# Performance work log

Hardware: AMD Instinct MI355X
Metric: run time of the kernel (lower is better)

Reference implementation:

```python
import jax, jax.numpy as jnp
import numpy as np

B, N, C, K = 16, 2000, 4, 8
EPS = 1e-5


def setup_inputs() -> dict:
    key = jax.random.key(0)
    ks = jax.random.split(key, 10)
    def p(k, shape, s=0.1):
        return jax.random.normal(k, shape, jnp.float32) * s
    return {
        "data": jax.random.normal(ks[0], (B, 1, N, C), jnp.float32),
        "x": jax.random.normal(ks[1], (B, 1, N, 4), jnp.float32),
        "w1a": p(ks[2], (128, C)), "b1a": jnp.zeros((128,), jnp.float32),
        "w1b": p(ks[3], (128, 128)), "b1b": jnp.zeros((128,), jnp.float32),
        "w2": p(ks[4], (128, 2 * C + 2)), "b2": jnp.zeros((128,), jnp.float32),
        "res_wa": p(ks[5], (4, 128, 128)), "res_ba": jnp.zeros((4, 128), jnp.float32),
        "res_wb": p(ks[6], (4, 128, 128)), "res_bb": jnp.zeros((4, 128), jnp.float32),
        "wl": p(ks[7], (1, 128)), "bl": jnp.zeros((1,), jnp.float32),
    }


def conv1x1(t, w, b):
    # t: [B, Cin, H, W], w: [Cout, Cin]
    return jnp.einsum('bchw,oc->bohw', t, w) + b[None, :, None, None]


def bn(t):
    # training-mode BatchNorm2d, gamma=1 beta=0 (default init)
    m = jnp.mean(t, axis=(0, 2, 3), keepdims=True)
    v = jnp.var(t, axis=(0, 2, 3), keepdims=True)
    return (t - m) * jax.lax.rsqrt(v + EPS)


def instn(t):
    # InstanceNorm2d, affine=False
    m = jnp.mean(t, axis=(2, 3), keepdims=True)
    v = jnp.var(t, axis=(2, 3), keepdims=True)
    return (t - m) * jax.lax.rsqrt(v + EPS)


def res_block(t, wa, ba, wb, bb):
    h = jax.nn.relu(bn(instn(conv1x1(t, wa, ba))))
    h = bn(instn(conv1x1(h, wb, bb)))
    return jax.nn.relu(h + t)


def knn_idx(f, k):
    # f: [B, D, N]; negative squared distance, top-(k+1), drop self
    xx = jnp.sum(f * f, axis=1)                        # [B, N]
    inner = jnp.einsum('bdn,bdm->bnm', f, f)           # [B, N, N]
    pd = 2.0 * inner - xx[:, :, None] - xx[:, None, :]
    idx = jax.lax.top_k(pd, k + 1)[1]                  # [B, N, k+1]
    return idx[:, :, 1:]


def graph_feature(f, idx):
    # f: [B, D, N], idx: [B, N, k] -> [B, 2D, N, k]
    xf = jnp.transpose(f, (0, 2, 1))                   # [B, N, D]
    nb = jax.vmap(lambda a, i: a[i])(xf, idx)          # [B, N, k, D]
    xt = xf[:, :, None, :]
    gf = jnp.concatenate([jnp.broadcast_to(xt, nb.shape), xt - nb], axis=-1)
    return jnp.transpose(gf, (0, 3, 1, 2))


def reference(data, x, w1a, b1a, w1b, b1b, w2, b2,
              res_wa, res_ba, res_wb, res_bb, wl, bl):
    n = data.shape[2]
    t = jnp.transpose(data, (0, 3, 2, 1))              # [B, C, N, 1]

    # self_attention
    h = conv1x1(t, w1a, b1a)
    h = jax.nn.relu(bn(h))
    h = conv1x1(h, w1b, b1b)[..., 0]                   # [B, 128, N]
    h = h / (jnp.linalg.norm(h, axis=1, keepdims=True) + 1e-5)
    A_rowsum = jnp.einsum('bcn,bcm->bm', h, h)         # sum_i A[i, j]
    D = (A_rowsum - 1.0) / n                           # [B, N] (eye subtraction)
    feat = jnp.concatenate(
        [t, jax.nn.relu(jnp.tanh(D))[:, None, :, None]], axis=1)  # [B, C+1, N, 1]

    f = feat[..., 0]                                   # [B, C+1, N]
    idx = knn_idx(f, K)
    g = graph_feature(f, idx)                          # [B, 2C+2, N, K]

    out = jax.nn.relu(bn(conv1x1(g, w2, b2)))          # [B, 128, N, K]
    out = jnp.max(out, axis=-1, keepdims=True)         # [B, 128, N, 1]

    for i in range(4):
        out = res_block(out, res_wa[i], res_ba[i], res_wb[i], res_bb[i])

    logit = conv1x1(out, wl, bl)[:, 0, :, 0]           # [B, N]

    # weighted 8-point
    weights = jax.nn.relu(jnp.tanh(logit))             # [B, N]
    xp = jnp.transpose(x[:, 0], (0, 2, 1))             # [B, 4, N]
    ones = jnp.ones_like(xp[:, 0])
    X = jnp.stack([xp[:, 2] * xp[:, 0], xp[:, 2] * xp[:, 1], xp[:, 2],
                   xp[:, 3] * xp[:, 0], xp[:, 3] * xp[:, 1], xp[:, 3],
                   xp[:, 0], xp[:, 1], ones], axis=1)  # [B, 9, N]
    X = jnp.transpose(X, (0, 2, 1))                    # [B, N, 9]
    XwX = jnp.einsum('bnp,bnq->bpq', X, weights[:, :, None] * X)  # [B, 9, 9]
    _, v = jnp.linalg.eigh(XwX)                        # ascending eigvals
    e_hat = v[:, :, 0]                                 # smallest-eig eigenvector
    e_hat = e_hat / jnp.linalg.norm(e_hat, axis=1, keepdims=True)

    return (D, logit, e_hat)
```

## Files before the change

kernel.cpp:

```cpp
#include <hip/hip_runtime.h>
#include <math.h>

#define BB 16
#define NN 2000
#define CH 128
#define KNN 8
#define JCH 8
#define JSZ 250

__device__ inline float wred(float v) {
    for (int off = 32; off > 0; off >>= 1) v += __shfl_down(v, off, 64);
    return v;
}

__global__ void k_build_t(const float* __restrict__ data, float* __restrict__ t) {
    int i = blockIdx.x * 256 + threadIdx.x;
    if (i >= BB * 4 * NN) return;
    int n = i % NN;
    int c = (i / NN) & 3;
    int b = i / (4 * NN);
    t[i] = data[(b * NN + n) * 4 + c];
}

__global__ void k_conv1(const float* __restrict__ t, const float* __restrict__ w1a,
                        const float* __restrict__ b1a, float* __restrict__ c1) {
    int i = blockIdx.x * 256 + threadIdx.x;
    if (i >= BB * CH * NN) return;
    int n = i % NN;
    int rest = i / NN;
    int o = rest & 127;
    int b = rest >> 7;
    float acc = b1a[o];
    for (int c = 0; c < 4; ++c) acc += w1a[o * 4 + c] * t[(b * 4 + c) * NN + n];
    c1[i] = acc;
}

__global__ void k_chanstats(const float* __restrict__ src, float* __restrict__ chAB) {
    int o = blockIdx.x;
    int tid = threadIdx.x;
    float s = 0.f, ss = 0.f;
    for (int b = 0; b < BB; ++b) {
        const float* p = src + (b * CH + o) * NN;
        for (int n = tid; n < NN; n += 256) { float v = p[n]; s += v; ss += v * v; }
    }
    s = wred(s); ss = wred(ss);
    __shared__ float sh[8];
    int wid = tid >> 6, lane = tid & 63;
    if (lane == 0) { sh[wid] = s; sh[4 + wid] = ss; }
    __syncthreads();
    if (tid == 0) {
        float S0 = sh[0] + sh[1] + sh[2] + sh[3];
        float SS = sh[4] + sh[5] + sh[6] + sh[7];
        float m = S0 / (float)(BB * NN);
        float var = SS / (float)(BB * NN) - m * m;
        float a = rsqrtf(var + 1e-5f);
        chAB[o] = a;
        chAB[CH + o] = -m * a;
    }
}

__global__ __launch_bounds__(256) void k_gemm(const float* __restrict__ X, const float* __restrict__ W,
                                              const float* __restrict__ bias, float* __restrict__ Y,
                                              const float* __restrict__ ab, int mode) {
    int ot = blockIdx.x, by = blockIdx.y;
    int b = by >> 5, nt = by & 31;
    int n0 = nt * 64, o0 = ot * 64;
    int tid = threadIdx.x;
    int tx = tid & 15, ty = tid >> 4;
    __shared__ float Xs[32][64];
    __shared__ float Ws[32][68];
    float acc[4][4] = {};
    for (int jc = 0; jc < 4; ++jc) {
        for (int q = 0; q < 8; ++q) {
            int e = q * 256 + tid;
            int jj = e >> 6, nn = e & 63;
            int j = jc * 32 + jj, n = n0 + nn;
            float v = 0.f;
            if (n < NN) {
                v = X[(b * CH + j) * NN + n];
                if (mode == 1) v = fmaxf(ab[j] * v + ab[CH + j], 0.f);
                else if (mode == 2) { int bc = b * CH + j; v = fmaxf(ab[bc * 2] * v + ab[bc * 2 + 1], 0.f); }
            }
            Xs[jj][nn] = v;
        }
        for (int q = 0; q < 8; ++q) {
            int e = q * 256 + tid;
            int jj = e & 31, oo = e >> 5;
            Ws[jj][oo] = W[(o0 + oo) * CH + jc * 32 + jj];
        }
        __syncthreads();
        for (int jj = 0; jj < 32; ++jj) {
            float4 wv = *(const float4*)&Ws[jj][ty * 4];
            float4 xv = *(const float4*)&Xs[jj][tx * 4];
            float wva[4] = {wv.x, wv.y, wv.z, wv.w};
            float xva[4] = {xv.x, xv.y, xv.z, xv.w};
#pragma unroll
            for (int a = 0; a < 4; ++a)
#pragma unroll
                for (int bq = 0; bq < 4; ++bq) acc[a][bq] += wva[a] * xva[bq];
        }
        __syncthreads();
    }
    for (int a = 0; a < 4; ++a) {
        int o = o0 + ty * 4 + a;
        float bi = bias[o];
        for (int q = 0; q < 4; ++q) {
            int n = n0 + tx * 4 + q;
            if (n < NN) Y[(b * CH + o) * NN + n] = acc[a][q] + bi;
        }
    }
}

__global__ void k_invn(const float* __restrict__ h2, float* __restrict__ invn) {
    int b = blockIdx.x >> 3, chunk = blockIdx.x & 7;
    int n = chunk * 256 + threadIdx.x;
    if (n >= NN) return;
    float acc = 0.f;
    for (int c = 0; c < CH; ++c) { float v = h2[(b * CH + c) * NN + n]; acc += v * v; }
    invn[b * NN + n] = 1.f / (sqrtf(acc) + 1e-5f);
}

__global__ void k_S(const float* __restrict__ h2, const float* __restrict__ invn, float* __restrict__ Sv) {
    int row = blockIdx.x;
    int b = row >> 7;
    const float* p = h2 + row * NN;
    const float* iv = invn + b * NN;
    float s = 0.f;
    for (int n = threadIdx.x; n < NN; n += 256) s += p[n] * iv[n];
    s = wred(s);
    __shared__ float sh[4];
    int wid = threadIdx.x >> 6, lane = threadIdx.x & 63;
    if (lane == 0) sh[wid] = s;
    __syncthreads();
    if (threadIdx.x == 0) Sv[row] = sh[0] + sh[1] + sh[2] + sh[3];
}

__global__ void k_Df(const float* __restrict__ h2, const float* __restrict__ invn,
                     const float* __restrict__ Sv, const float* __restrict__ t,
                     float* __restrict__ outD, float* __restrict__ f5) {
    int b = blockIdx.x >> 3, chunk = blockIdx.x & 7;
    int n = chunk * 256 + threadIdx.x;
    if (n >= NN) return;
    float acc = 0.f;
    for (int c = 0; c < CH; ++c) acc += h2[(b * CH + c) * NN + n] * Sv[b * CH + c];
    float Ar = acc * invn[b * NN + n];
    float Dv = (Ar - 1.0f) / (float)NN;
    outD[b * NN + n] = Dv;
    for (int c = 0; c < 4; ++c) f5[(b * 5 + c) * NN + n] = t[(b * 4 + c) * NN + n];
    f5[(b * 5 + 4) * NN + n] = fmaxf(tanhf(Dv), 0.f);
}

__global__ __launch_bounds__(256) void k_knn_part(const float* __restrict__ f5,
                                                  float* __restrict__ pd, int* __restrict__ pj) {
    __shared__ float4 fs4[JSZ];
    __shared__ float fs1[JSZ];
    int jc = blockIdx.x, ic = blockIdx.y, b = blockIdx.z;
    int j0 = jc * JSZ;
    int tid = threadIdx.x;
    const float* fb = f5 + b * 5 * NN;
    for (int e = tid; e < JSZ; e += 256) {
        float4 v;
        v.x = fb[0 * NN + j0 + e];
        v.y = fb[1 * NN + j0 + e];
        v.z = fb[2 * NN + j0 + e];
        v.w = fb[3 * NN + j0 + e];
        fs4[e] = v;
        fs1[e] = fb[4 * NN + j0 + e];
    }
    __syncthreads();
    int i = ic * 256 + tid;
    if (i >= NN) return;
    float fi0 = fb[i], fi1 = fb[NN + i], fi2 = fb[2 * NN + i], fi3 = fb[3 * NN + i], fi4 = fb[4 * NN + i];
    float bd[8]; int bj[8];
#pragma unroll
    for (int q = 0; q < 8; ++q) { bd[q] = 1e30f; bj[q] = 0x7fffffff; }
    for (int jj = 0; jj < JSZ; ++jj) {
        float4 fj = fs4[jj];
        float fj4 = fs1[jj];
        int j = j0 + jj;
        float d0 = fi0 - fj.x, d1 = fi1 - fj.y, d2 = fi2 - fj.z;
        float d3 = fi3 - fj.w, d4 = fi4 - fj4;
        float d = d0 * d0 + d1 * d1 + d2 * d2 + d3 * d3 + d4 * d4;
        if (j != i && d < bd[7]) {
            float cd = d; int cj = j;
#pragma unroll
            for (int q = 0; q < 8; ++q) {
                bool lt = cd < bd[q];
                float td = lt ? bd[q] : cd;
                int tj = lt ? bj[q] : cj;
                bd[q] = lt ? cd : bd[q];
                bj[q] = lt ? cj : bj[q];
                cd = td; cj = tj;
            }
        }
    }
    long base = ((long)(b * NN + i) * JCH + jc) * 8;
#pragma unroll
    for (int q = 0; q < 8; ++q) { pd[base + q] = bd[q]; pj[base + q] = bj[q]; }
}

__global__ __launch_bounds__(256) void k_knn_merge(const float* __restrict__ pd, const int* __restrict__ pj,
                                                   int* __restrict__ idxb) {
    int s = blockIdx.x * 256 + threadIdx.x;
    if (s >= BB * NN) return;
    const float* dl = pd + (long)s * JCH * 8;
    const int* jl = pj + (long)s * JCH * 8;
    int ptr[JCH];
#pragma unroll
    for (int c = 0; c < JCH; ++c) ptr[c] = 0;
    for (int q = 0; q < 8; ++q) {
        float best = 1e38f; int bestj = 0x7fffffff; int bc = 0;
#pragma unroll
        for (int c = 0; c < JCH; ++c) {
            if (ptr[c] < 8) {
                float d = dl[c * 8 + ptr[c]];
                int j = jl[c * 8 + ptr[c]];
                if (d < best || (d == best && j < bestj)) { best = d; bestj = j; bc = c; }
            }
        }
        idxb[s * 8 + q] = bestj;
        ++ptr[bc];
    }
}

__global__ __launch_bounds__(256) void k_gstats(const float* __restrict__ f5, const int* __restrict__ idxb,
                                                double* __restrict__ gacc) {
    int s = blockIdx.x * 256 + threadIdx.x;
    float acc[65];
#pragma unroll
    for (int q = 0; q < 65; ++q) acc[q] = 0.f;
    if (s < BB * NN) {
        int b = s / NN, n = s - b * NN;
        float fo[5];
#pragma unroll
        for (int c = 0; c < 5; ++c) fo[c] = f5[(b * 5 + c) * NN + n];
        float sd[5] = {0, 0, 0, 0, 0};
        float sdd[15];
#pragma unroll
        for (int q = 0; q < 15; ++q) sdd[q] = 0.f;
        for (int k = 0; k < 8; ++k) {
            int j = idxb[s * 8 + k];
            float df[5];
#pragma unroll
            for (int c = 0; c < 5; ++c) df[c] = fo[c] - f5[(b * 5 + c) * NN + j];
#pragma unroll
            for (int c = 0; c < 5; ++c) sd[c] += df[c];
            int t = 0;
#pragma unroll
            for (int c = 0; c < 5; ++c)
#pragma unroll
                for (int d2 = c; d2 < 5; ++d2) { sdd[t] += df[c] * df[d2]; ++t; }
        }
#pragma unroll
        for (int c = 0; c < 5; ++c) { acc[c] = 8.f * fo[c]; acc[5 + c] = sd[c]; }
        int t = 10, sc = 0;
        for (int p = 0; p < 10; ++p)
            for (int q = p; q < 10; ++q) {
                float v;
                if (q < 5) v = 8.f * fo[p] * fo[q];
                else if (p < 5) v = fo[p] * sd[q - 5];
                else { v = sdd[sc]; ++sc; }
                acc[t++] = v;
            }
    }
#pragma unroll 1
    for (int q = 0; q < 65; ++q) {
        float v = acc[q];
        for (int off = 32; off > 0; off >>= 1) v += __shfl_down(v, off, 64);
        acc[q] = v;
    }
    __shared__ float sh[4][65];
    int lane = threadIdx.x & 63, wid = threadIdx.x >> 6;
    if (lane == 0) {
        for (int q = 0; q < 65; ++q) sh[wid][q] = acc[q];
    }
    __syncthreads();
    if (threadIdx.x < 65) {
        float tot = sh[0][threadIdx.x] + sh[1][threadIdx.x] + sh[2][threadIdx.x] + sh[3][threadIdx.x];
        atomicAdd(&gacc[threadIdx.x], (double)tot);
    }
}

__global__ void k_gfinal(const double* __restrict__ gacc, const float* __restrict__ w2,
                         const float* __restrict__ b2, float* __restrict__ g2ab) {
    int o = threadIdx.x;
    if (o >= 128) return;
    double inv = 1.0 / (double)(BB * NN * 8);
    double Wr[10];
    for (int c = 0; c < 10; ++c) Wr[c] = (double)w2[o * 10 + c];
    double gm[10];
    for (int c = 0; c < 10; ++c) gm[c] = gacc[c] * inv;
    double b0 = (double)b2[o];
    double mean = b0;
    for (int c = 0; c < 10; ++c) mean += Wr[c] * gm[c];
    double e2 = b0 * b0 + 2.0 * b0 * (mean - b0);
    int t = 10;
    for (int p = 0; p < 10; ++p)
        for (int q = p; q < 10; ++q) {
            double G = gacc[t] * inv; ++t;
            double contrib = Wr[p] * Wr[q] * G;
            e2 += (p == q) ? contrib : 2.0 * contrib;
        }
    double var = e2 - mean * mean;
    double a = 1.0 / sqrt(var + 1e-5);
    g2ab[o] = (float)a;
    g2ab[128 + o] = (float)(-mean * a);
}

__global__ __launch_bounds__(256) void k_graphconv(const float* __restrict__ f5, const int* __restrict__ idxb,
                                                   const float* __restrict__ w2, const float* __restrict__ b2,
                                                   const float* __restrict__ g2ab, float* __restrict__ x0) {
    __shared__ float ws[1280], bs[128];
    __shared__ float fo_s[16][5], fnb_s[16][8][5];
    __shared__ int idxs[16][8];
    int b = blockIdx.x / 125, tile = blockIdx.x % 125;
    int nbase = tile * 16;
    int tid = threadIdx.x;
    for (int e = tid; e < 1280; e += 256) ws[e] = w2[e];
    if (tid < 128) bs[tid] = b2[tid];
    if (tid < 128) { int nn = tid >> 3, k = tid & 7; idxs[nn][k] = idxb[(b * NN + nbase + nn) * 8 + k]; }
    if (tid >= 128 && tid < 208) { int e = tid - 128; int nn = e / 5, c = e % 5; fo_s[nn][c] = f5[(b * 5 + c) * NN + nbase + nn]; }
    __syncthreads();
    for (int e = tid; e < 640; e += 256) {
        int nn = e / 40, r = e % 40, k = r / 5, c = r % 5;
        fnb_s[nn][k][c] = f5[(b * 5 + c) * NN + idxs[nn][k]];
    }
    __syncthreads();
    int nn = tid & 15, og = tid >> 4;
    float fo[5];
#pragma unroll
    for (int c = 0; c < 5; ++c) fo[c] = fo_s[nn][c];
    for (int oo = 0; oo < 8; ++oo) {
        int o = og * 8 + oo;
        float base = bs[o];
        float wn[5];
#pragma unroll
        for (int c = 0; c < 5; ++c) {
            float w1 = ws[o * 10 + c], w5 = ws[o * 10 + 5 + c];
            base += (w1 + w5) * fo[c];
            wn[c] = w5;
        }
        float mx = -1e30f;
        for (int k = 0; k < 8; ++k) {
            float v = base;
#pragma unroll
            for (int c = 0; c < 5; ++c) v -= wn[c] * fnb_s[nn][k][c];
            mx = fmaxf(mx, v);
        }
        float y = fmaxf(g2ab[o] * mx + g2ab[128 + o], 0.f);
        x0[(b * CH + o) * NN + nbase + nn] = y;
    }
}

__global__ void k_rowstats(const float* __restrict__ src, float* __restrict__ stats) {
    int row = blockIdx.x;
    const float* p = src + row * NN;
    float s = 0.f, ss = 0.f;
    for (int n = threadIdx.x; n < NN; n += 256) { float v = p[n]; s += v; ss += v * v; }
    s = wred(s); ss = wred(ss);
    __shared__ float sh[8];
    int wid = threadIdx.x >> 6, lane = threadIdx.x & 63;
    if (lane == 0) { sh[wid] = s; sh[4 + wid] = ss; }
    __syncthreads();
    if (threadIdx.x == 0) {
        float S0 = sh[0] + sh[1] + sh[2] + sh[3];
        float SS = sh[4] + sh[5] + sh[6] + sh[7];
        float m = S0 / (float)NN;
        float var = SS / (float)NN - m * m;
        stats[row * 2] = m;
        stats[row * 2 + 1] = var;
    }
}

__global__ void k_finalize(const float* __restrict__ stats, float* __restrict__ ab) {
    int c = threadIdx.x;
    if (c >= 128) return;
    float acc = 0.f;
    for (int b = 0; b < BB; ++b) { float var = stats[(b * CH + c) * 2 + 1]; acc += var / (var + 1e-5f); }
    float vc = acc / (float)BB;
    float sc = rsqrtf(vc + 1e-5f);
    for (int b = 0; b < BB; ++b) {
        float m = stats[(b * CH + c) * 2];
        float var = stats[(b * CH + c) * 2 + 1];
        float a = rsqrtf(var + 1e-5f) * sc;
        ab[(b * CH + c) * 2] = a;
        ab[(b * CH + c) * 2 + 1] = -m * a;
    }
}

__global__ void k_resadd(const float* __restrict__ Bm, const float* __restrict__ ab,
                         const float* __restrict__ x, float* __restrict__ y) {
    int i = blockIdx.x * 256 + threadIdx.x;
    if (i >= BB * CH * NN) return;
    int bc = i / NN;
    float v = ab[bc * 2] * Bm[i] + ab[bc * 2 + 1] + x[i];
    y[i] = fmaxf(v, 0.f);
}

__global__ void k_logit(const float* __restrict__ x4, const float* __restrict__ wl,
                        const float* __restrict__ bl, float* __restrict__ outLogit) {
    int b = blockIdx.x >> 3, chunk = blockIdx.x & 7;
    int n = chunk * 256 + threadIdx.x;
    if (n >= NN) return;
    float acc = 0.f;
    for (int c = 0; c < CH; ++c) acc += wl[c] * x4[(b * CH + c) * NN + n];
    outLogit[b * NN + n] = acc + bl[0];
}

__global__ __launch_bounds__(256) void k_xwx(const float* __restrict__ logit, const float* __restrict__ x_in,
                                             float* __restrict__ XwX) {
    int b = blockIdx.x;
    int tid = threadIdx.x;
    float a[45];
#pragma unroll
    for (int q = 0; q < 45; ++q) a[q] = 0.f;
    for (int n = tid; n < NN; n += 256) {
        float lg = logit[b * NN + n];
        float w = fmaxf(tanhf(lg), 0.f);
        const float* xp = x_in + (b * NN + n) * 4;
        float px = xp[0], py = xp[1], z = xp[2], wq = xp[3];
        float X9[9] = {z * px, z * py, z, wq * px, wq * py, wq, px, py, 1.f};
        int t = 0;
#pragma unroll
        for (int p = 0; p < 9; ++p) {
            float wp = w * X9[p];
#pragma unroll
            for (int q = p; q < 9; ++q) { a[t] += wp * X9[q]; ++t; }
        }
    }
#pragma unroll 1
    for (int q = 0; q < 45; ++q) {
        float v = a[q];
        for (int off = 32; off > 0; off >>= 1) v += __shfl_down(v, off, 64);
        a[q] = v;
    }
    __shared__ float sh[4][45];
    int lane = tid & 63, wid = tid >> 6;
    if (lane == 0) {
        for (int q = 0; q < 45; ++q) sh[wid][q] = a[q];
    }
    __syncthreads();
    if (tid < 45) XwX[b * 45 + tid] = sh[0][tid] + sh[1][tid] + sh[2][tid] + sh[3][tid];
}

__device__ inline float slapy2_f(float x, float y) {
    float xa = fabsf(x), ya = fabsf(y);
    float w = fmaxf(xa, ya), z = fminf(xa, ya);
    if (z == 0.f) return w;
    float q = z / w;
    return w * sqrtf(1.f + q * q);
}

__device__ inline void slartg_f(float f, float g, float& c, float& s, float& r) {
    if (g == 0.f) { c = 1.f; s = 0.f; r = f; }
    else if (f == 0.f) { c = 0.f; s = (g > 0.f ? 1.f : -1.f); r = fabsf(g); }
    else {
        float d = sqrtf(f * f + g * g);
        c = fabsf(f) / d;
        r = (f >= 0.f) ? d : -d;
        s = g / r;
    }
}

__device__ void slaev2_f(float a, float b, float c, float& rt1, float& rt2, float& cs1, float& sn1) {
    float sm = a + c, df = a - c;
    float adf = fabsf(df), tb = b + b, ab = fabsf(tb);
    float acmx, acmn;
    if (fabsf(a) > fabsf(c)) { acmx = a; acmn = c; } else { acmx = c; acmn = a; }
    float rt;
    if (adf > ab) { float q = ab / adf; rt = adf * sqrtf(1.f + q * q); }
    else if (adf < ab) { float q = adf / ab; rt = ab * sqrtf(1.f + q * q); }
    else rt = ab * sqrtf(2.f);
    int sgn1;
    if (sm < 0.f) { rt1 = 0.5f * (sm - rt); sgn1 = -1; rt2 = (acmx / rt1) * acmn - (b / rt1) * b; }
    else if (sm > 0.f) { rt1 = 0.5f * (sm + rt); sgn1 = 1; rt2 = (acmx / rt1) * acmn - (b / rt1) * b; }
    else { rt1 = 0.5f * rt; rt2 = -0.5f * rt; sgn1 = 1; }
    float cs; int sgn2;
    if (df >= 0.f) { cs = df + rt; sgn2 = 1; } else { cs = df - rt; sgn2 = -1; }
    float acs = fabsf(cs);
    if (acs > ab) {
        float ct = -tb / cs;
        sn1 = 1.f / sqrtf(1.f + ct * ct);
        cs1 = ct * sn1;
    } else {
        if (ab == 0.f) { cs1 = 1.f; sn1 = 0.f; }
        else { float tn = -cs / tb; cs1 = 1.f / sqrtf(1.f + tn * tn); sn1 = tn * cs1; }
    }
    if (sgn1 == sgn2) { float tn = cs1; cs1 = -sn1; sn1 = tn; }
}

__global__ __launch_bounds__(64) void k_eigh(const float* __restrict__ XwX, float* __restrict__ out_e) {
    __shared__ float Am[81];
    __shared__ float Zm[81];
    int bb = blockIdx.x;
    if (threadIdx.x != 0) return;
#define AA(i, j) Am[(i) * 9 + (j)]
#define ZZ(i, j) Zm[(i) * 9 + (j)]
    {
        const float* src = XwX + bb * 45;
        int t = 0;
        for (int p = 0; p < 9; ++p)
            for (int q = p; q < 9; ++q) { float v = src[t++]; AA(p, q) = v; AA(q, p) = v; }
    }
    float d[9], e[9], tau[9];
    for (int i = 0; i < 8; ++i) {
        float alpha = AA(i + 1, i);
        float xn2 = 0.f;
        for (int j = i + 2; j < 9; ++j) xn2 += AA(j, i) * AA(j, i);
        float taui;
        if (xn2 == 0.f) { taui = 0.f; e[i] = alpha; }
        else {
            float xnorm = sqrtf(xn2);
            float beta = slapy2_f(alpha, xnorm);
            beta = (alpha >= 0.f) ? -beta : beta;
            taui = (beta - alpha) / beta;
            float scl = 1.f / (alpha - beta);
            for (int j = i + 2; j < 9; ++j) AA(j, i) *= scl;
            e[i] = beta;
            float p[9], w[9];
            for (int j = i + 1; j < 9; ++j) {
                float acc = AA(j, i + 1);
                for (int k2 = i + 2; k2 < 9; ++k2) acc += AA(j, k2) * AA(k2, i);
                p[j] = taui * acc;
            }
            float dot = p[i + 1];
            for (int j = i + 2; j < 9; ++j) dot += p[j] * AA(j, i);
            float alpha2 = -0.5f * taui * dot;
            w[i + 1] = p[i + 1] + alpha2;
            for (int j = i + 2; j < 9; ++j) w[j] = p[j] + alpha2 * AA(j, i);
            for (int j = i + 1; j < 9; ++j) {
                float vj = (j == i + 1) ? 1.f : AA(j, i);
                for (int k2 = i + 1; k2 < 9; ++k2) {
                    float vk = (k2 == i + 1) ? 1.f : AA(k2, i);
                    AA(j, k2) -= vj * w[k2] + w[j] * vk;
                }
            }
        }
        tau[i] = taui;
    }
    for (int i = 0; i < 9; ++i) d[i] = AA(i, i);
    for (int i = 0; i < 81; ++i) Zm[i] = 0.f;
    for (int i = 0; i < 9; ++i) ZZ(i, i) = 1.f;
    const float eps = 5.9604645e-08f;
    const float eps2 = 3.5527137e-15f;
    const float safmin = 1.17549435e-38f;
    const int n = 9;
    int nmaxit = n * 30, jtot = 0;
    int l1 = 0;
    while (l1 <= n - 1) {
        if (l1 > 0) e[l1 - 1] = 0.f;
        int m = n - 1;
        for (int mm = l1; mm <= n - 2; ++mm) {
            float tst = fabsf(e[mm]);
            if (tst == 0.f) { m = mm; break; }
            if (tst <= (sqrtf(fabsf(d[mm])) * sqrtf(fabsf(d[mm + 1]))) * eps) { e[mm] = 0.f; m = mm; break; }
        }
        int l = l1, lsv = l, lend = m, lendsv = lend;
        l1 = m + 1;
        if (lend == l) continue;
        if (fabsf(d[lend]) < fabsf(d[l])) { lend = lsv; l = lendsv; }
        if (lend > l) {
            for (;;) {
                int m2 = lend;
                if (l != lend) {
                    for (int mm = l; mm <= lend - 1; ++mm) {
                        float tst = e[mm] * e[mm];
                        if (tst <= (eps2 * fabsf(d[mm])) * fabsf(d[mm + 1]) + safmin) { m2 = mm; break; }
                    }
                }
                if (m2 < lend) e[m2] = 0.f;
                float p = d[l];
                if (m2 == l) { d[l] = p; ++l; if (l <= lend) continue; else break; }
                if (m2 == l + 1) {
                    float rt1, rt2, c, s;
                    slaev2_f(d[l], e[l], d[l + 1], rt1, rt2, c, s);
                    for (int r2 = 0; r2 < 9; ++r2) {
                        float tmp = ZZ(r2, l + 1);
                        ZZ(r2, l + 1) = c * tmp - s * ZZ(r2, l);
                        ZZ(r2, l) = s * tmp + c * ZZ(r2, l);
                    }
                    d[l] = rt1; d[l + 1] = rt2; e[l] = 0.f; l += 2;
                    if (l <= lend) continue; else break;
                }
                if (jtot == nmaxit) break;
                ++jtot;
                float g = (d[l + 1] - p) / (2.f * e[l]);
                float r = slapy2_f(g, 1.f);
                g = d[m2] - p + e[l] / (g + (g >= 0.f ? fabsf(r) : -fabsf(r)));
                float s = 1.f, c = 1.f;
                p = 0.f;
                float csv[9], snv[9];
                for (int i = m2 - 1; i >= l; --i) {
                    float f = s * e[i], bq = c * e[i];
                    slartg_f(g, f, c, s, r);
                    if (i != m2 - 1) e[i + 1] = r;
                    g = d[i + 1] - p;
                    r = (d[i] - g) * s + 2.f * c * bq;
                    p = s * r;
                    d[i + 1] = g + p;
                    g = c * r - bq;
                    csv[i] = c; snv[i] = -s;
                }
                for (int jj = m2 - 1; jj >= l; --jj) {
                    float cj = csv[jj], sj = snv[jj];
                    for (int r2 = 0; r2 < 9; ++r2) {
                        float tmp = ZZ(r2, jj + 1);
                        ZZ(r2, jj + 1) = cj * tmp - sj * ZZ(r2, jj);
                        ZZ(r2, jj) = sj * tmp + cj * ZZ(r2, jj);
                    }
                }
                d[l] -= p; e[l] = g;
            }
        } else {
            for (;;) {
                int m2 = lend;
                if (l != lend) {
                    for (int mm = l; mm >= lend + 1; --mm) {
                        float tst = e[mm - 1] * e[mm - 1];
                        if (tst <= (eps2 * fabsf(d[mm])) * fabsf(d[mm - 1]) + safmin) { m2 = mm; break; }
                    }
                }
                if (m2 > lend) e[m2 - 1] = 0.f;
                float p = d[l];
                if (m2 == l) { d[l] = p; --l; if (l >= lend) continue; else break; }
                if (m2 == l - 1) {
                    float rt1, rt2, c, s;
                    slaev2_f(d[l - 1], e[l - 1], d[l], rt1, rt2, c, s);
                    for (int r2 = 0; r2 < 9; ++r2) {
                        float tmp = ZZ(r2, l);
                        ZZ(r2, l) = c * tmp - s * ZZ(r2, l - 1);
                        ZZ(r2, l - 1) = s * tmp + c * ZZ(r2, l - 1);
                    }
                    d[l - 1] = rt1; d[l] = rt2; e[l - 1] = 0.f; l -= 2;
                    if (l >= lend) continue; else break;
                }
                if (jtot == nmaxit) break;
                ++jtot;
                float g = (d[l - 1] - p) / (2.f * e[l - 1]);
                float r = slapy2_f(g, 1.f);
                g = d[m2] - p + e[l - 1] / (g + (g >= 0.f ? fabsf(r) : -fabsf(r)));
                float s = 1.f, c = 1.f;
                p = 0.f;
                float csv[9], snv[9];
                for (int i = m2; i <= l - 1; ++i) {
                    float f = s * e[i], bq = c * e[i];
                    slartg_f(g, f, c, s, r);
                    if (i != m2) e[i - 1] = r;
                    g = d[i] - p;
                    r = (d[i + 1] - g) * s + 2.f * c * bq;
                    p = s * r;
                    d[i] = g + p;
                    g = c * r - bq;
                    csv[i] = c; snv[i] = s;
                }
                for (int jj = m2; jj <= l - 1; ++jj) {
                    float cj = csv[jj], sj = snv[jj];
                    for (int r2 = 0; r2 < 9; ++r2) {
                        float tmp = ZZ(r2, jj + 1);
                        ZZ(r2, jj + 1) = cj * tmp - sj * ZZ(r2, jj);
                        ZZ(r2, jj) = sj * tmp + cj * ZZ(r2, jj);
                    }
                }
                d[l] -= p; e[l - 1] = g;
            }
        }
    }
    for (int ii = 1; ii < 9; ++ii) {
        int i = ii - 1, kk = i;
        float p = d[i];
        for (int j = ii; j < 9; ++j)
            if (d[j] < p) { kk = j; p = d[j]; }
        if (kk != i) {
            d[kk] = d[i]; d[i] = p;
            for (int r2 = 0; r2 < 9; ++r2) { float tmp = ZZ(r2, i); ZZ(r2, i) = ZZ(r2, kk); ZZ(r2, kk) = tmp; }
        }
    }
    float v0[9];
    for (int r2 = 0; r2 < 9; ++r2) v0[r2] = ZZ(r2, 0);
    for (int i = 7; i >= 0; --i) {
        float ti = tau[i];
        if (ti == 0.f) continue;
        float dot = v0[i + 1];
        for (int j = i + 2; j < 9; ++j) dot += AA(j, i) * v0[j];
        dot *= ti;
        v0[i + 1] -= dot;
        for (int j = i + 2; j < 9; ++j) v0[j] -= AA(j, i) * dot;
    }
    float nrm = 0.f;
    for (int r2 = 0; r2 < 9; ++r2) nrm += v0[r2] * v0[r2];
    nrm = sqrtf(nrm);
    for (int r2 = 0; r2 < 9; ++r2) out_e[bb * 9 + r2] = v0[r2] / nrm;
#undef AA
#undef ZZ
}

extern "C" void kernel_launch(void* const* d_in, const int* in_sizes, int n_in,
                              void* d_out, int out_size, void* d_ws, size_t ws_size,
                              hipStream_t stream) {
    const float* data = (const float*)d_in[0];
    const float* x_in = (const float*)d_in[1];
    const float* w1a = (const float*)d_in[2];
    const float* b1a = (const float*)d_in[3];
    const float* w1b = (const float*)d_in[4];
    const float* b1b = (const float*)d_in[5];
    const float* w2 = (const float*)d_in[6];
    const float* b2 = (const float*)d_in[7];
    const float* res_wa = (const float*)d_in[8];
    const float* res_ba = (const float*)d_in[9];
    const float* res_wb = (const float*)d_in[10];
    const float* res_bb = (const float*)d_in[11];
    const float* wl = (const float*)d_in[12];
    const float* bl = (const float*)d_in[13];
    float* out = (float*)d_out;

    double* gacc = (double*)d_ws;
    float* xwx = (float*)((char*)d_ws + 1024);
    float* fbase = (float*)((char*)d_ws + 8192);
    float* big0 = fbase;
    float* big1 = big0 + BB * CH * NN;
    float* big2 = big1 + BB * CH * NN;
    float* tbuf = big2 + BB * CH * NN;
    float* f5 = tbuf + BB * 4 * NN;
    float* invn = f5 + BB * 5 * NN;
    float* Sv = invn + BB * NN;
    int* idxb = (int*)(Sv + BB * CH);
    float* chAB = (float*)(idxb + BB * NN * 8);
    float* stA = chAB + 256;
    float* abA = stA + BB * CH * 2;
    float* stB = abA + BB * CH * 2;
    float* abB = stB + BB * CH * 2;
    float* g2ab = abB + BB * CH * 2;
    float* knn_pd = big2;
    int* knn_pj = (int*)(big2 + BB * NN * JCH * 8);

    hipMemsetAsync(d_ws, 0, 1024, stream);

    k_build_t<<<500, 256, 0, stream>>>(data, tbuf);
    k_conv1<<<16000, 256, 0, stream>>>(tbuf, w1a, b1a, big0);
    k_chanstats<<<128, 256, 0, stream>>>(big0, chAB);
    k_gemm<<<dim3(2, 512), 256, 0, stream>>>(big0, w1b, b1b, big1, chAB, 1);
    k_invn<<<128, 256, 0, stream>>>(big1, invn);
    k_S<<<2048, 256, 0, stream>>>(big1, invn, Sv);
    k_Df<<<128, 256, 0, stream>>>(big1, invn, Sv, tbuf, out, f5);
    k_knn_part<<<dim3(JCH, 8, BB), 256, 0, stream>>>(f5, knn_pd, knn_pj);
    k_knn_merge<<<125, 256, 0, stream>>>(knn_pd, knn_pj, idxb);
    k_gstats<<<125, 256, 0, stream>>>(f5, idxb, gacc);
    k_gfinal<<<1, 128, 0, stream>>>(gacc, w2, b2, g2ab);
    k_graphconv<<<2000, 256, 0, stream>>>(f5, idxb, w2, b2, g2ab, big0);

    float* xb = big0;
    float* hb = big1;
    for (int i = 0; i < 4; ++i) {
        k_gemm<<<dim3(2, 512), 256, 0, stream>>>(xb, res_wa + i * CH * CH, res_ba + i * CH, hb, nullptr, 0);
        k_rowstats<<<2048, 256, 0, stream>>>(hb, stA);
        k_finalize<<<1, 128, 0, stream>>>(stA, abA);
        k_gemm<<<dim3(2, 512), 256, 0, stream>>>(hb, res_wb + i * CH * CH, res_bb + i * CH, big2, abA, 2);
        k_rowstats<<<2048, 256, 0, stream>>>(big2, stB);
        k_finalize<<<1, 128, 0, stream>>>(stB, abB);
        k_resadd<<<16000, 256, 0, stream>>>(big2, abB, xb, hb);
        float* tmp = xb; xb = hb; hb = tmp;
    }

    k_logit<<<128, 256, 0, stream>>>(xb, wl, bl, out + BB * NN);
    k_xwx<<<16, 256, 0, stream>>>(out + BB * NN, x_in, xwx);
    k_eigh<<<16, 64, 0, stream>>>(xwx, out + 2 * BB * NN);
}
```

Before: 866.3 us.

## Log QL rotations and backapply to single eigenvector instead of full Z

Result: faster. 843.7 us (-2.6%).

```diff
diff --git a/kernel.cpp b/kernel.cpp
--- a/kernel.cpp
+++ b/kernel.cpp
@@ -489,20 +489,26 @@
     if (sgn1 == sgn2) { float tn = cs1; cs1 = -sn1; sn1 = tn; }
 }
 
+#define ROTLOG_MAX 2560
+
 __global__ __launch_bounds__(64) void k_eigh(const float* __restrict__ XwX, float* __restrict__ out_e) {
     __shared__ float Am[81];
-    __shared__ float Zm[81];
+    __shared__ float dsh[9], esh[9], tsh[9];
+    __shared__ float rc[ROTLOG_MAX], rs[ROTLOG_MAX];
+    __shared__ int rj[ROTLOG_MAX];
     int bb = blockIdx.x;
     if (threadIdx.x != 0) return;
+    float* d = dsh;
+    float* e = esh;
+    float* tau = tsh;
+    int cnt = 0;
 #define AA(i, j) Am[(i) * 9 + (j)]
-#define ZZ(i, j) Zm[(i) * 9 + (j)]
     {
         const float* src = XwX + bb * 45;
         int t = 0;
         for (int p = 0; p < 9; ++p)
             for (int q = p; q < 9; ++q) { float v = src[t++]; AA(p, q) = v; AA(q, p) = v; }
     }
-    float d[9], e[9], tau[9];
     for (int i = 0; i < 8; ++i) {
         float alpha = AA(i + 1, i);
         float xn2 = 0.f;
@@ -539,8 +545,6 @@
         tau[i] = taui;
     }
     for (int i = 0; i < 9; ++i) d[i] = AA(i, i);
-    for (int i = 0; i < 81; ++i) Zm[i] = 0.f;
-    for (int i = 0; i < 9; ++i) ZZ(i, i) = 1.f;
     const float eps = 5.9604645e-08f;
     const float eps2 = 3.5527137e-15f;
     const float safmin = 1.17549435e-38f;
@@ -574,11 +578,7 @@
                 if (m2 == l + 1) {
                     float rt1, rt2, c, s;
                     slaev2_f(d[l], e[l], d[l + 1], rt1, rt2, c, s);
-                    for (int r2 = 0; r2 < 9; ++r2) {
-                        float tmp = ZZ(r2, l + 1);
-                        ZZ(r2, l + 1) = c * tmp - s * ZZ(r2, l);
-                        ZZ(r2, l) = s * tmp + c * ZZ(r2, l);
-                    }
+                    rc[cnt] = c; rs[cnt] = s; rj[cnt] = l; ++cnt;
                     d[l] = rt1; d[l + 1] = rt2; e[l] = 0.f; l += 2;
                     if (l <= lend) continue; else break;
                 }
@@ -589,7 +589,6 @@
                 g = d[m2] - p + e[l] / (g + (g >= 0.f ? fabsf(r) : -fabsf(r)));
                 float s = 1.f, c = 1.f;
                 p = 0.f;
-                float csv[9], snv[9];
                 for (int i = m2 - 1; i >= l; --i) {
                     float f = s * e[i], bq = c * e[i];
                     slartg_f(g, f, c, s, r);
@@ -599,15 +598,7 @@
                     p = s * r;
                     d[i + 1] = g + p;
                     g = c * r - bq;
-                    csv[i] = c; snv[i] = -s;
-                }
-                for (int jj = m2 - 1; jj >= l; --jj) {
-                    float cj = csv[jj], sj = snv[jj];
-                    for (int r2 = 0; r2 < 9; ++r2) {
-                        float tmp = ZZ(r2, jj + 1);
-                        ZZ(r2, jj + 1) = cj * tmp - sj * ZZ(r2, jj);
-                        ZZ(r2, jj) = sj * tmp + cj * ZZ(r2, jj);
-                    }
+                    rc[cnt] = c; rs[cnt] = -s; rj[cnt] = i; ++cnt;
                 }
                 d[l] -= p; e[l] = g;
             }
@@ -626,11 +617,7 @@
                 if (m2 == l - 1) {
                     float rt1, rt2, c, s;
                     slaev2_f(d[l - 1], e[l - 1], d[l], rt1, rt2, c, s);
-                    for (int r2 = 0; r2 < 9; ++r2) {
-                        float tmp = ZZ(r2, l);
-                        ZZ(r2, l) = c * tmp - s * ZZ(r2, l - 1);
-                        ZZ(r2, l - 1) = s * tmp + c * ZZ(r2, l - 1);
-                    }
+                    rc[cnt] = c; rs[cnt] = s; rj[cnt] = l - 1; ++cnt;
                     d[l - 1] = rt1; d[l] = rt2; e[l - 1] = 0.f; l -= 2;
                     if (l >= lend) continue; else break;
                 }
@@ -641,7 +628,6 @@
                 g = d[m2] - p + e[l - 1] / (g + (g >= 0.f ? fabsf(r) : -fabsf(r)));
                 float s = 1.f, c = 1.f;
                 p = 0.f;
-                float csv[9], snv[9];
                 for (int i = m2; i <= l - 1; ++i) {
                     float f = s * e[i], bq = c * e[i];
                     slartg_f(g, f, c, s, r);
@@ -651,20 +637,14 @@
                     p = s * r;
                     d[i] = g + p;
                     g = c * r - bq;
-                    csv[i] = c; snv[i] = s;
-                }
-                for (int jj = m2; jj <= l - 1; ++jj) {
-                    float cj = csv[jj], sj = snv[jj];
-                    for (int r2 = 0; r2 < 9; ++r2) {
-                        float tmp = ZZ(r2, jj + 1);
-                        ZZ(r2, jj + 1) = cj * tmp - sj * ZZ(r2, jj);
-                        ZZ(r2, jj) = sj * tmp + cj * ZZ(r2, jj);
-                    }
+                    rc[cnt] = c; rs[cnt] = s; rj[cnt] = i; ++cnt;
                 }
                 d[l] -= p; e[l - 1] = g;
             }
         }
     }
+    int perm[9];
+    for (int i = 0; i < 9; ++i) perm[i] = i;
     for (int ii = 1; ii < 9; ++ii) {
         int i = ii - 1, kk = i;
         float p = d[i];
@@ -672,11 +652,28 @@
             if (d[j] < p) { kk = j; p = d[j]; }
         if (kk != i) {
             d[kk] = d[i]; d[i] = p;
-            for (int r2 = 0; r2 < 9; ++r2) { float tmp = ZZ(r2, i); ZZ(r2, i) = ZZ(r2, kk); ZZ(r2, kk) = tmp; }
-        }
-    }
-    float v0[9];
-    for (int r2 = 0; r2 < 9; ++r2) v0[r2] = ZZ(r2, 0);
+            int tp = perm[i]; perm[i] = perm[kk]; perm[kk] = tp;
+        }
+    }
+    int kcol = perm[0];
+    float w0 = (kcol == 0) ? 1.f : 0.f, w1 = (kcol == 1) ? 1.f : 0.f, w2 = (kcol == 2) ? 1.f : 0.f;
+    float w3 = (kcol == 3) ? 1.f : 0.f, w4 = (kcol == 4) ? 1.f : 0.f, w5 = (kcol == 5) ? 1.f : 0.f;
+    float w6 = (kcol == 6) ? 1.f : 0.f, w7 = (kcol == 7) ? 1.f : 0.f, w8 = (kcol == 8) ? 1.f : 0.f;
+    for (int t = cnt - 1; t >= 0; --t) {
+        float c = rc[t], s = rs[t];
+        int j = rj[t];
+        switch (j) {
+            case 0: { float a = w0, b = w1; w0 = c * a - s * b; w1 = s * a + c * b; } break;
+            case 1: { float a = w1, b = w2; w1 = c * a - s * b; w2 = s * a + c * b; } break;
+            case 2: { float a = w2, b = w3; w2 = c * a - s * b; w3 = s * a + c * b; } break;
+            case 3: { float a = w3, b = w4; w3 = c * a - s * b; w4 = s * a + c * b; } break;
+            case 4: { float a = w4, b = w5; w4 = c * a - s * b; w5 = s * a + c * b; } break;
+            case 5: { float a = w5, b = w6; w5 = c * a - s * b; w6 = s * a + c * b; } break;
+            case 6: { float a = w6, b = w7; w6 = c * a - s * b; w7 = s * a + c * b; } break;
+            default: { float a = w7, b = w8; w7 = c * a - s * b; w8 = s * a + c * b; } break;
+        }
+    }
+    float v0[9] = {w0, w1, w2, w3, w4, w5, w6, w7, w8};
     for (int i = 7; i >= 0; --i) {
         float ti = tau[i];
         if (ti == 0.f) continue;
@@ -691,7 +688,6 @@
     nrm = sqrtf(nrm);
     for (int r2 = 0; r2 < 9; ++r2) out_e[bb * 9 + r2] = v0[r2] / nrm;
 #undef AA
-#undef ZZ
 }
 
 extern "C" void kernel_launch(void* const* d_in, const int* in_sizes, int n_in,
```
